# Kernel tuning notes

Hardware: AMD Instinct MI355X
Metric: run time of the kernel (lower is better)

## Reference

```python
import jax, jax.numpy as jnp
import numpy as np

B, H, W = 2, 512, 512
C2, HEADS = 128, 8
EPS_NORM = 1e-12  # torch F.normalize eps


def conv2d(x, w, groups=1):
    # x: NCHW, w: OIHW, stride 1, SAME padding
    return jax.lax.conv_general_dilated(
        x, w, window_strides=(1, 1), padding='SAME',
        dimension_numbers=('NCHW', 'OIHW', 'NCHW'),
        feature_group_count=groups)


def setup_inputs() -> dict:
    key = jax.random.key(0)
    ks = jax.random.split(key, 7)
    x = jax.random.normal(ks[0], (B, 2, H, W), dtype=jnp.float32)
    e = jax.random.normal(ks[1], (B, 1, H, W), dtype=jnp.float32)
    # imhead: 1x1 conv 2 -> 2*C2, then 3x3 depthwise conv on 2*C2 channels
    w_conv1 = jax.random.normal(ks[2], (2 * C2, 2, 1, 1), dtype=jnp.float32) * 0.5
    w_dw = jax.random.normal(ks[3], (2 * C2, 1, 3, 3), dtype=jnp.float32) * 0.2
    # ehead: 3x3 conv 1 -> C2 (groups=1)
    w_ehead = jax.random.normal(ks[4], (C2, 1, 3, 3), dtype=jnp.float32) * 0.2
    # project_out: 1x1 conv C2 -> 2
    w_proj = jax.random.normal(ks[5], (2, C2, 1, 1), dtype=jnp.float32) * 0.1
    a1 = jnp.ones((HEADS, 1, 1), dtype=jnp.float32)
    return {"x": x, "e": e, "w_conv1": w_conv1, "w_dw": w_dw,
            "w_ehead": w_ehead, "w_proj": w_proj, "a1": a1}


def l2norm_lastdim(t):
    n = jnp.sqrt(jnp.sum(t * t, axis=-1, keepdims=True))
    return t / jnp.maximum(n, EPS_NORM)


def reference(x, e, w_conv1, w_dw, w_ehead, w_proj, a1):
    b, _, h, w = x.shape
    # NOTE: attHead_image.forward never applies its LayerNorm, so neither do we.
    q1 = conv2d(x, w_conv1)                 # (B, 2*C2, H, W)
    q1 = conv2d(q1, w_dw, groups=2 * C2)    # depthwise 3x3
    k_eg = conv2d(e, w_ehead)               # (B, C2, H, W)
    q_im, v_im = jnp.split(q1, 2, axis=1)   # each (B, C2, H, W)

    def heads(t):  # (B, C2, H, W) -> (B, head, c, H*W)
        return t.reshape(b, HEADS, C2 // HEADS, h * w)

    q = l2norm_lastdim(heads(q_im))
    k = l2norm_lastdim(heads(k_eg))
    v = heads(v_im)

    # channel-wise attention: (B, head, c, c)
    attn = jnp.einsum('bhcn,bhdn->bhcd', q, k) * a1
    attn = jax.nn.softmax(attn, axis=-1)
    out = jnp.einsum('bhcd,bhdn->bhcn', attn, v)  # (B, head, c, H*W)
    out = out.reshape(b, C2, h, w)
    return x + conv2d(out, w_proj)
```

## Files before the change

### kernel.cpp

```cpp
#include <hip/hip_runtime.h>

#define IMG 512
#define NPIX (IMG*IMG)

__global__ __launch_bounds__(256,2) void gram_kernel(const float* __restrict__ x,
                                                     const float* __restrict__ e,
                                                     float* __restrict__ part){
  const int dyi = blockIdx.y;
  const int dy  = dyi - 2;
  const int b   = blockIdx.z;
  const int half= threadIdx.x >> 7;
  const int cx  = (threadIdx.x & 127) << 2;
  const int r0  = (blockIdx.x << 4) + (half << 3);
  const float* x0 = x + (size_t)b*2*NPIX;
  const float* x1 = x0 + NPIX;
  const float* ep = e + (size_t)b*NPIX;

  float acc[6][5];
#pragma unroll
  for (int t=0;t<6;t++)
#pragma unroll
    for (int j=0;j<5;j++) acc[t][j]=0.f;

  const bool okL = (cx >= 4), okR = (cx < 508);

#pragma unroll 2
  for (int s=0;s<8;s++){
    const int r = r0+s;
    const float4 a0 = *(const float4*)(x0 + r*IMG + cx);
    const float4 a1 = *(const float4*)(x1 + r*IMG + cx);
    const float4 aE = *(const float4*)(ep + r*IMG + cx);
    const int rb = r+dy;
    if ((unsigned)rb < (unsigned)IMG){
      const float* p0 = x0 + rb*IMG;
      const float* p1 = x1 + rb*IMG;
      const float* pe = ep + rb*IMG;
      float w0[8], w1[8], wE[8];
      {
        const float4 z = make_float4(0.f,0.f,0.f,0.f);
        float4 L,M,R;
        L = okL ? *(const float4*)(p0+cx-4) : z;
        M = *(const float4*)(p0+cx);
        R = okR ? *(const float4*)(p0+cx+4) : z;
        w0[0]=L.z;w0[1]=L.w;w0[2]=M.x;w0[3]=M.y;w0[4]=M.z;w0[5]=M.w;w0[6]=R.x;w0[7]=R.y;
        L = okL ? *(const float4*)(p1+cx-4) : z;
        M = *(const float4*)(p1+cx);
        R = okR ? *(const float4*)(p1+cx+4) : z;
        w1[0]=L.z;w1[1]=L.w;w1[2]=M.x;w1[3]=M.y;w1[4]=M.z;w1[5]=M.w;w1[6]=R.x;w1[7]=R.y;
        L = okL ? *(const float4*)(pe+cx-4) : z;
        M = *(const float4*)(pe+cx);
        R = okR ? *(const float4*)(pe+cx+4) : z;
        wE[0]=L.z;wE[1]=L.w;wE[2]=M.x;wE[3]=M.y;wE[4]=M.z;wE[5]=M.w;wE[6]=R.x;wE[7]=R.y;
      }
#pragma unroll
      for (int j=0;j<5;j++){
        acc[0][j] += a0.x*w0[j] + a0.y*w0[j+1] + a0.z*w0[j+2] + a0.w*w0[j+3];
        acc[1][j] += a0.x*w1[j] + a0.y*w1[j+1] + a0.z*w1[j+2] + a0.w*w1[j+3];
        acc[2][j] += a1.x*w1[j] + a1.y*w1[j+1] + a1.z*w1[j+2] + a1.w*w1[j+3];
        acc[3][j] += a0.x*wE[j] + a0.y*wE[j+1] + a0.z*wE[j+2] + a0.w*wE[j+3];
        acc[4][j] += a1.x*wE[j] + a1.y*wE[j+1] + a1.z*wE[j+2] + a1.w*wE[j+3];
        acc[5][j] += aE.x*wE[j] + aE.y*wE[j+1] + aE.z*wE[j+2] + aE.w*wE[j+3];
      }
    }
  }

  __shared__ float red[4][30];
  const int wv   = threadIdx.x >> 6;
  const int lane = threadIdx.x & 63;
#pragma unroll
  for (int t=0;t<6;t++)
#pragma unroll
    for (int j=0;j<5;j++){
      float v = acc[t][j];
      for (int off=32; off; off>>=1) v += __shfl_down(v, off);
      if (lane==0) red[wv][t*5+j] = v;
    }
  __syncthreads();
  if (threadIdx.x < 30){
    const int g = b*5 + dyi;
    part[(size_t)((g*32)+blockIdx.x)*32 + threadIdx.x] =
      red[0][threadIdx.x]+red[1][threadIdx.x]+red[2][threadIdx.x]+red[3][threadIdx.x];
  }
}

__global__ __launch_bounds__(256,1) void attn_kernel(const float* __restrict__ part,
                                                     const float* __restrict__ w_conv1,
                                                     const float* __restrict__ w_dw,
                                                     const float* __restrict__ w_ehead,
                                                     const float* __restrict__ w_proj,
                                                     const float* __restrict__ a1,
                                                     float* __restrict__ AB){
  const int tid = threadIdx.x;
  __shared__ float Lred[2][150];
  __shared__ float we_lds[128][9];
  __shared__ float nk_lds[2][128];
  __shared__ float attn_lds[2][8][16][16];
  __shared__ float M_lds[2][2][128];

  for (int i=tid; i<300; i+=256){
    const int bb=i/150, li=i%150;
    const int t=li/25, lag=li%25, dyi=lag/5, dxi=lag%5;
    const int g = bb*5+dyi;
    const float* p = part + (size_t)(g*32)*32 + t*5+dxi;
    float s=0.f;
#pragma unroll
    for (int j=0;j<32;j++) s += p[j*32];
    Lred[bb][li]=s;
  }
  if (tid<128){
#pragma unroll
    for (int t=0;t<9;t++) we_lds[tid][t]=w_ehead[tid*9+t];
  }
  __syncthreads();

  const int b=tid>>7, h=(tid>>4)&7, c=tid&15;
  const int C=h*16+c;
  const float* Lb  = Lred[b];
  const float* L00=Lb, *L01=Lb+25, *L11=Lb+50, *L0e=Lb+75, *L1e=Lb+100, *Lee=Lb+125;

  float u[9], v[9];
  {
    const float wa=w_conv1[C*2+0], wb=w_conv1[C*2+1];
#pragma unroll
    for (int t=0;t<9;t++){ const float wd=w_dw[C*9+t]; u[t]=wd*wa; v[t]=wd*wb; }
  }
  float nq2=0.f, nk2=0.f;
#pragma unroll
  for (int t=0;t<9;t++){
    const int ty=t/3, tx=t%3;
#pragma unroll
    for (int t2=0;t2<9;t2++){
      const int dy=t2/3-ty, dx=t2%3-tx;
      const int di=( dy+2)*5+( dx+2);
      const int dj=(-dy+2)*5+(-dx+2);
      nq2 += u[t]*u[t2]*L00[di] + u[t]*v[t2]*L01[di] + v[t]*u[t2]*L01[dj] + v[t]*v[t2]*L11[di];
      nk2 += we_lds[C][t]*we_lds[C][t2]*Lee[di];
    }
  }
  nk_lds[b][C]=sqrtf(nk2);
  float P[9];
#pragma unroll
  for (int t2=0;t2<9;t2++){
    float s=0.f;
    const int t2y=t2/3, t2x=t2%3;
#pragma unroll
    for (int t=0;t<9;t++){
      const int di=(t2y-t/3+2)*5+(t2x-t%3+2);
      s += u[t]*L0e[di] + v[t]*L1e[di];
    }
    P[t2]=s;
  }
  __syncthreads();
  const float inv_nq = 1.f/fmaxf(sqrtf(nq2), 1e-12f);
  const float a1h=a1[h];
  float lg[16], mx=-1e30f;
#pragma unroll
  for (int d=0; d<16; d++){
    float S=0.f;
#pragma unroll
    for (int t2=0;t2<9;t2++) S += P[t2]*we_lds[h*16+d][t2];
    const float l = S*inv_nq/fmaxf(nk_lds[b][h*16+d],1e-12f)*a1h;
    lg[d]=l; mx=fmaxf(mx,l);
  }
  float sum=0.f;
#pragma unroll
  for (int d=0;d<16;d++){ lg[d]=expf(lg[d]-mx); sum+=lg[d]; }
  const float inv=1.f/sum;
#pragma unroll
  for (int d=0;d<16;d++) attn_lds[b][h][c][d]=lg[d]*inv;
  __syncthreads();
  for (int i=tid;i<512;i+=256){
    const int G=i&127, o=(i>>7)&1, bb=i>>8;
    const int hh=G>>4, dd=G&15;
    float s=0.f;
#pragma unroll
    for (int cc=0;cc<16;cc++) s += w_proj[o*128 + hh*16+cc]*attn_lds[bb][hh][cc][dd];
    M_lds[bb][o][G]=s;
  }
  __syncthreads();
  if (tid<36){
    const int t=tid%9, o=(tid/9)&1, bb=tid/18;
    float sa=0.f, sb=0.f;
    for (int G=0;G<128;G++){
      const float m=M_lds[bb][o][G];
      const float wd=w_dw[(128+G)*9+t];
      sa += m*wd*w_conv1[(128+G)*2+0];
      sb += m*wd*w_conv1[(128+G)*2+1];
    }
    AB[(bb*2+o)*9+t]      = sa;
    AB[72 + (bb*2+o)*9+t] = sb;
  }
}

__global__ __launch_bounds__(256,1) void out_kernel(const float* __restrict__ x,
                                                    const float* __restrict__ AB,
                                                    float* __restrict__ out){
  const int idx = blockIdx.x*256 + threadIdx.x;
  const int b  = idx >> 16;
  const int y  = (idx >> 7) & (IMG-1);
  const int xc = (idx & 127) << 2;
  const float* x0 = x + (size_t)b*2*NPIX;
  const float* x1 = x0 + NPIX;

  float A0[9],A1[9],B0[9],B1[9];
#pragma unroll
  for (int t=0;t<9;t++){
    A0[t]=AB[(b*2+0)*9+t];      A1[t]=AB[(b*2+1)*9+t];
    B0[t]=AB[72+(b*2+0)*9+t];   B1[t]=AB[72+(b*2+1)*9+t];
  }
  float v0[3][6], v1[3][6];
#pragma unroll
  for (int r=0;r<3;r++){
    const int yy=y-1+r;
    if ((unsigned)yy < (unsigned)IMG){
      const float* p0=x0+(size_t)yy*IMG;
      const float* p1=x1+(size_t)yy*IMG;
      const float4 m0=*(const float4*)(p0+xc);
      const float4 m1=*(const float4*)(p1+xc);
      v0[r][1]=m0.x; v0[r][2]=m0.y; v0[r][3]=m0.z; v0[r][4]=m0.w;
      v1[r][1]=m1.x; v1[r][2]=m1.y; v1[r][3]=m1.z; v1[r][4]=m1.w;
      v0[r][0]=(xc>0)?p0[xc-1]:0.f;        v1[r][0]=(xc>0)?p1[xc-1]:0.f;
      v0[r][5]=(xc+4<IMG)?p0[xc+4]:0.f;    v1[r][5]=(xc+4<IMG)?p1[xc+4]:0.f;
    } else {
#pragma unroll
      for (int c2=0;c2<6;c2++){v0[r][c2]=0.f;v1[r][c2]=0.f;}
    }
  }
  float res0[4], res1[4];
#pragma unroll
  for (int i=0;i<4;i++){
    float s0=v0[1][i+1];
    float s1=v1[1][i+1];
#pragma unroll
    for (int t=0;t<9;t++){
      const int ty=t/3, tx=t%3;
      const float g0=v0[ty][i+tx], g1=v1[ty][i+tx];
      s0 += A0[t]*g0 + B0[t]*g1;
      s1 += A1[t]*g0 + B1[t]*g1;
    }
    res0[i]=s0; res1[i]=s1;
  }
  float* o0p = out + ((size_t)(b*2+0)*IMG + y)*IMG + xc;
  float* o1p = out + ((size_t)(b*2+1)*IMG + y)*IMG + xc;
  *(float4*)o0p = make_float4(res0[0],res0[1],res0[2],res0[3]);
  *(float4*)o1p = make_float4(res1[0],res1[1],res1[2],res1[3]);
}

extern "C" void kernel_launch(void* const* d_in, const int* in_sizes, int n_in,
                              void* d_out, int out_size, void* d_ws, size_t ws_size,
                              hipStream_t stream){
  const float* x       = (const float*)d_in[0];
  const float* e       = (const float*)d_in[1];
  const float* w_conv1 = (const float*)d_in[2];
  const float* w_dw    = (const float*)d_in[3];
  const float* w_ehead = (const float*)d_in[4];
  const float* w_proj  = (const float*)d_in[5];
  const float* a1      = (const float*)d_in[6];
  float* ws   = (float*)d_ws;
  float* part = ws;
  float* AB   = ws + 10240;
  float* out  = (float*)d_out;

  hipLaunchKernelGGL(gram_kernel, dim3(32,5,2), dim3(256), 0, stream, x, e, part);
  hipLaunchKernelGGL(attn_kernel, dim3(1),      dim3(256), 0, stream, part,
                     w_conv1, w_dw, w_ehead, w_proj, a1, AB);
  hipLaunchKernelGGL(out_kernel,  dim3(512),    dim3(256), 0, stream, x, AB, out);
}
```

Measured before the change: 44.82 us.

## Fuse gram, attention and output kernels into one persistent kernel with grid barrier

```diff
diff --git a/kernel.cpp b/kernel.cpp
--- a/kernel.cpp
+++ b/kernel.cpp
@@ -2,248 +2,259 @@
 
 #define IMG 512
 #define NPIX (IMG*IMG)
-
-__global__ __launch_bounds__(256,2) void gram_kernel(const float* __restrict__ x,
-                                                     const float* __restrict__ e,
-                                                     float* __restrict__ part){
-  const int dyi = blockIdx.y;
-  const int dy  = dyi - 2;
-  const int b   = blockIdx.z;
-  const int half= threadIdx.x >> 7;
-  const int cx  = (threadIdx.x & 127) << 2;
-  const int r0  = (blockIdx.x << 4) + (half << 3);
-  const float* x0 = x + (size_t)b*2*NPIX;
-  const float* x1 = x0 + NPIX;
-  const float* ep = e + (size_t)b*NPIX;
-
-  float acc[6][5];
-#pragma unroll
-  for (int t=0;t<6;t++)
-#pragma unroll
-    for (int j=0;j<5;j++) acc[t][j]=0.f;
-
-  const bool okL = (cx >= 4), okR = (cx < 508);
-
-#pragma unroll 2
-  for (int s=0;s<8;s++){
-    const int r = r0+s;
-    const float4 a0 = *(const float4*)(x0 + r*IMG + cx);
-    const float4 a1 = *(const float4*)(x1 + r*IMG + cx);
-    const float4 aE = *(const float4*)(ep + r*IMG + cx);
-    const int rb = r+dy;
-    if ((unsigned)rb < (unsigned)IMG){
-      const float* p0 = x0 + rb*IMG;
-      const float* p1 = x1 + rb*IMG;
-      const float* pe = ep + rb*IMG;
-      float w0[8], w1[8], wE[8];
-      {
-        const float4 z = make_float4(0.f,0.f,0.f,0.f);
-        float4 L,M,R;
-        L = okL ? *(const float4*)(p0+cx-4) : z;
-        M = *(const float4*)(p0+cx);
-        R = okR ? *(const float4*)(p0+cx+4) : z;
-        w0[0]=L.z;w0[1]=L.w;w0[2]=M.x;w0[3]=M.y;w0[4]=M.z;w0[5]=M.w;w0[6]=R.x;w0[7]=R.y;
-        L = okL ? *(const float4*)(p1+cx-4) : z;
-        M = *(const float4*)(p1+cx);
-        R = okR ? *(const float4*)(p1+cx+4) : z;
-        w1[0]=L.z;w1[1]=L.w;w1[2]=M.x;w1[3]=M.y;w1[4]=M.z;w1[5]=M.w;w1[6]=R.x;w1[7]=R.y;
-        L = okL ? *(const float4*)(pe+cx-4) : z;
-        M = *(const float4*)(pe+cx);
-        R = okR ? *(const float4*)(pe+cx+4) : z;
-        wE[0]=L.z;wE[1]=L.w;wE[2]=M.x;wE[3]=M.y;wE[4]=M.z;wE[5]=M.w;wE[6]=R.x;wE[7]=R.y;
-      }
-#pragma unroll
-      for (int j=0;j<5;j++){
-        acc[0][j] += a0.x*w0[j] + a0.y*w0[j+1] + a0.z*w0[j+2] + a0.w*w0[j+3];
-        acc[1][j] += a0.x*w1[j] + a0.y*w1[j+1] + a0.z*w1[j+2] + a0.w*w1[j+3];
-        acc[2][j] += a1.x*w1[j] + a1.y*w1[j+1] + a1.z*w1[j+2] + a1.w*w1[j+3];
-        acc[3][j] += a0.x*wE[j] + a0.y*wE[j+1] + a0.z*wE[j+2] + a0.w*wE[j+3];
-        acc[4][j] += a1.x*wE[j] + a1.y*wE[j+1] + a1.z*wE[j+2] + a1.w*wE[j+3];
-        acc[5][j] += aE.x*wE[j] + aE.y*wE[j+1] + aE.z*wE[j+2] + aE.w*wE[j+3];
-      }
-    }
-  }
+#define NBLK 256
+
+__global__ __launch_bounds__(256,2) void fused_kernel(
+    const float* __restrict__ x, const float* __restrict__ e,
+    const float* __restrict__ w_conv1, const float* __restrict__ w_dw,
+    const float* __restrict__ w_ehead, const float* __restrict__ w_proj,
+    const float* __restrict__ a1,
+    float* __restrict__ part, unsigned int* __restrict__ bar,
+    float* __restrict__ out)
+{
+  const int blk = blockIdx.x;
+  const int tid = threadIdx.x;
 
   __shared__ float red[4][30];
-  const int wv   = threadIdx.x >> 6;
-  const int lane = threadIdx.x & 63;
-#pragma unroll
-  for (int t=0;t<6;t++)
-#pragma unroll
-    for (int j=0;j<5;j++){
-      float v = acc[t][j];
-      for (int off=32; off; off>>=1) v += __shfl_down(v, off);
-      if (lane==0) red[wv][t*5+j] = v;
-    }
-  __syncthreads();
-  if (threadIdx.x < 30){
-    const int g = b*5 + dyi;
-    part[(size_t)((g*32)+blockIdx.x)*32 + threadIdx.x] =
-      red[0][threadIdx.x]+red[1][threadIdx.x]+red[2][threadIdx.x]+red[3][threadIdx.x];
-  }
-}
-
-__global__ __launch_bounds__(256,1) void attn_kernel(const float* __restrict__ part,
-                                                     const float* __restrict__ w_conv1,
-                                                     const float* __restrict__ w_dw,
-                                                     const float* __restrict__ w_ehead,
-                                                     const float* __restrict__ w_proj,
-                                                     const float* __restrict__ a1,
-                                                     float* __restrict__ AB){
-  const int tid = threadIdx.x;
   __shared__ float Lred[2][150];
   __shared__ float we_lds[128][9];
   __shared__ float nk_lds[2][128];
   __shared__ float attn_lds[2][8][16][16];
   __shared__ float M_lds[2][2][128];
-
-  for (int i=tid; i<300; i+=256){
-    const int bb=i/150, li=i%150;
-    const int t=li/25, lag=li%25, dyi=lag/5, dxi=lag%5;
-    const int g = bb*5+dyi;
-    const float* p = part + (size_t)(g*32)*32 + t*5+dxi;
-    float s=0.f;
-#pragma unroll
-    for (int j=0;j<32;j++) s += p[j*32];
-    Lred[bb][li]=s;
-  }
-  if (tid<128){
-#pragma unroll
-    for (int t=0;t<9;t++) we_lds[tid][t]=w_ehead[tid*9+t];
+  __shared__ float AB_lds[2][2][2][9];
+
+  for (int u = blk; u < 320; u += NBLK){
+    const int bx  = u & 31;
+    const int dyi = (u >> 5) % 5;
+    const int dy  = dyi - 2;
+    const int b   = u / 160;
+    const int half= tid >> 7;
+    const int cx  = (tid & 127) << 2;
+    const int r0  = (bx << 4) + (half << 3);
+    const float* x0 = x + (size_t)b*2*NPIX;
+    const float* x1 = x0 + NPIX;
+    const float* ep = e + (size_t)b*NPIX;
+
+    float acc[6][5];
+#pragma unroll
+    for (int t=0;t<6;t++)
+#pragma unroll
+      for (int j=0;j<5;j++) acc[t][j]=0.f;
+
+    const bool okL = (cx >= 4), okR = (cx < 508);
+
+#pragma unroll 2
+    for (int s=0;s<8;s++){
+      const int r = r0+s;
+      const float4 a0 = *(const float4*)(x0 + r*IMG + cx);
+      const float4 a1v= *(const float4*)(x1 + r*IMG + cx);
+      const float4 aE = *(const float4*)(ep + r*IMG + cx);
+      const int rb = r+dy;
+      if ((unsigned)rb < (unsigned)IMG){
+        const float* p0 = x0 + rb*IMG;
+        const float* p1 = x1 + rb*IMG;
+        const float* pe = ep + rb*IMG;
+        float w0[8], w1[8], wE[8];
+        {
+          const float4 z = make_float4(0.f,0.f,0.f,0.f);
+          float4 L,M,R;
+          L = okL ? *(const float4*)(p0+cx-4) : z;
+          M = *(const float4*)(p0+cx);
+          R = okR ? *(const float4*)(p0+cx+4) : z;
+          w0[0]=L.z;w0[1]=L.w;w0[2]=M.x;w0[3]=M.y;w0[4]=M.z;w0[5]=M.w;w0[6]=R.x;w0[7]=R.y;
+          L = okL ? *(const float4*)(p1+cx-4) : z;
+          M = *(const float4*)(p1+cx);
+          R = okR ? *(const float4*)(p1+cx+4) : z;
+          w1[0]=L.z;w1[1]=L.w;w1[2]=M.x;w1[3]=M.y;w1[4]=M.z;w1[5]=M.w;w1[6]=R.x;w1[7]=R.y;
+          L = okL ? *(const float4*)(pe+cx-4) : z;
+          M = *(const float4*)(pe+cx);
+          R = okR ? *(const float4*)(pe+cx+4) : z;
+          wE[0]=L.z;wE[1]=L.w;wE[2]=M.x;wE[3]=M.y;wE[4]=M.z;wE[5]=M.w;wE[6]=R.x;wE[7]=R.y;
+        }
+#pragma unroll
+        for (int j=0;j<5;j++){
+          acc[0][j] += a0.x*w0[j] + a0.y*w0[j+1] + a0.z*w0[j+2] + a0.w*w0[j+3];
+          acc[1][j] += a0.x*w1[j] + a0.y*w1[j+1] + a0.z*w1[j+2] + a0.w*w1[j+3];
+          acc[2][j] += a1v.x*w1[j] + a1v.y*w1[j+1] + a1v.z*w1[j+2] + a1v.w*w1[j+3];
+          acc[3][j] += a0.x*wE[j] + a0.y*wE[j+1] + a0.z*wE[j+2] + a0.w*wE[j+3];
+          acc[4][j] += a1v.x*wE[j] + a1v.y*wE[j+1] + a1v.z*wE[j+2] + a1v.w*wE[j+3];
+          acc[5][j] += aE.x*wE[j] + aE.y*wE[j+1] + aE.z*wE[j+2] + aE.w*wE[j+3];
+        }
+      }
+    }
+
+    const int wv   = tid >> 6;
+    const int lane = tid & 63;
+#pragma unroll
+    for (int t=0;t<6;t++)
+#pragma unroll
+      for (int j=0;j<5;j++){
+        float v = acc[t][j];
+        for (int off=32; off; off>>=1) v += __shfl_down(v, off);
+        if (lane==0) red[wv][t*5+j] = v;
+      }
+    __syncthreads();
+    if (tid < 30)
+      part[(size_t)u*32 + tid] = red[0][tid]+red[1][tid]+red[2][tid]+red[3][tid];
+    __syncthreads();
+  }
+
+  if (tid == 0){
+    __threadfence();
+    __hip_atomic_fetch_add(bar, 1u, __ATOMIC_RELEASE, __HIP_MEMORY_SCOPE_AGENT);
+    while (__hip_atomic_load(bar, __ATOMIC_ACQUIRE, __HIP_MEMORY_SCOPE_AGENT) < NBLK) { }
   }
   __syncthreads();
 
-  const int b=tid>>7, h=(tid>>4)&7, c=tid&15;
-  const int C=h*16+c;
-  const float* Lb  = Lred[b];
-  const float* L00=Lb, *L01=Lb+25, *L11=Lb+50, *L0e=Lb+75, *L1e=Lb+100, *Lee=Lb+125;
-
-  float u[9], v[9];
   {
-    const float wa=w_conv1[C*2+0], wb=w_conv1[C*2+1];
-#pragma unroll
-    for (int t=0;t<9;t++){ const float wd=w_dw[C*9+t]; u[t]=wd*wa; v[t]=wd*wb; }
-  }
-  float nq2=0.f, nk2=0.f;
-#pragma unroll
-  for (int t=0;t<9;t++){
-    const int ty=t/3, tx=t%3;
-#pragma unroll
-    for (int t2=0;t2<9;t2++){
-      const int dy=t2/3-ty, dx=t2%3-tx;
-      const int di=( dy+2)*5+( dx+2);
-      const int dj=(-dy+2)*5+(-dx+2);
-      nq2 += u[t]*u[t2]*L00[di] + u[t]*v[t2]*L01[di] + v[t]*u[t2]*L01[dj] + v[t]*v[t2]*L11[di];
-      nk2 += we_lds[C][t]*we_lds[C][t2]*Lee[di];
-    }
-  }
-  nk_lds[b][C]=sqrtf(nk2);
-  float P[9];
-#pragma unroll
-  for (int t2=0;t2<9;t2++){
-    float s=0.f;
-    const int t2y=t2/3, t2x=t2%3;
-#pragma unroll
-    for (int t=0;t<9;t++){
-      const int di=(t2y-t/3+2)*5+(t2x-t%3+2);
-      s += u[t]*L0e[di] + v[t]*L1e[di];
-    }
-    P[t2]=s;
-  }
-  __syncthreads();
-  const float inv_nq = 1.f/fmaxf(sqrtf(nq2), 1e-12f);
-  const float a1h=a1[h];
-  float lg[16], mx=-1e30f;
-#pragma unroll
-  for (int d=0; d<16; d++){
-    float S=0.f;
-#pragma unroll
-    for (int t2=0;t2<9;t2++) S += P[t2]*we_lds[h*16+d][t2];
-    const float l = S*inv_nq/fmaxf(nk_lds[b][h*16+d],1e-12f)*a1h;
-    lg[d]=l; mx=fmaxf(mx,l);
-  }
-  float sum=0.f;
-#pragma unroll
-  for (int d=0;d<16;d++){ lg[d]=expf(lg[d]-mx); sum+=lg[d]; }
-  const float inv=1.f/sum;
-#pragma unroll
-  for (int d=0;d<16;d++) attn_lds[b][h][c][d]=lg[d]*inv;
-  __syncthreads();
-  for (int i=tid;i<512;i+=256){
-    const int G=i&127, o=(i>>7)&1, bb=i>>8;
-    const int hh=G>>4, dd=G&15;
-    float s=0.f;
-#pragma unroll
-    for (int cc=0;cc<16;cc++) s += w_proj[o*128 + hh*16+cc]*attn_lds[bb][hh][cc][dd];
-    M_lds[bb][o][G]=s;
-  }
-  __syncthreads();
-  if (tid<36){
-    const int t=tid%9, o=(tid/9)&1, bb=tid/18;
-    float sa=0.f, sb=0.f;
-    for (int G=0;G<128;G++){
-      const float m=M_lds[bb][o][G];
-      const float wd=w_dw[(128+G)*9+t];
-      sa += m*wd*w_conv1[(128+G)*2+0];
-      sb += m*wd*w_conv1[(128+G)*2+1];
-    }
-    AB[(bb*2+o)*9+t]      = sa;
-    AB[72 + (bb*2+o)*9+t] = sb;
-  }
-}
-
-__global__ __launch_bounds__(256,1) void out_kernel(const float* __restrict__ x,
-                                                    const float* __restrict__ AB,
-                                                    float* __restrict__ out){
-  const int idx = blockIdx.x*256 + threadIdx.x;
-  const int b  = idx >> 16;
-  const int y  = (idx >> 7) & (IMG-1);
-  const int xc = (idx & 127) << 2;
-  const float* x0 = x + (size_t)b*2*NPIX;
-  const float* x1 = x0 + NPIX;
-
-  float A0[9],A1[9],B0[9],B1[9];
-#pragma unroll
-  for (int t=0;t<9;t++){
-    A0[t]=AB[(b*2+0)*9+t];      A1[t]=AB[(b*2+1)*9+t];
-    B0[t]=AB[72+(b*2+0)*9+t];   B1[t]=AB[72+(b*2+1)*9+t];
-  }
-  float v0[3][6], v1[3][6];
-#pragma unroll
-  for (int r=0;r<3;r++){
-    const int yy=y-1+r;
-    if ((unsigned)yy < (unsigned)IMG){
-      const float* p0=x0+(size_t)yy*IMG;
-      const float* p1=x1+(size_t)yy*IMG;
-      const float4 m0=*(const float4*)(p0+xc);
-      const float4 m1=*(const float4*)(p1+xc);
-      v0[r][1]=m0.x; v0[r][2]=m0.y; v0[r][3]=m0.z; v0[r][4]=m0.w;
-      v1[r][1]=m1.x; v1[r][2]=m1.y; v1[r][3]=m1.z; v1[r][4]=m1.w;
-      v0[r][0]=(xc>0)?p0[xc-1]:0.f;        v1[r][0]=(xc>0)?p1[xc-1]:0.f;
-      v0[r][5]=(xc+4<IMG)?p0[xc+4]:0.f;    v1[r][5]=(xc+4<IMG)?p1[xc+4]:0.f;
-    } else {
-#pragma unroll
-      for (int c2=0;c2<6;c2++){v0[r][c2]=0.f;v1[r][c2]=0.f;}
-    }
-  }
-  float res0[4], res1[4];
-#pragma unroll
-  for (int i=0;i<4;i++){
-    float s0=v0[1][i+1];
-    float s1=v1[1][i+1];
+    for (int i=tid; i<300; i+=256){
+      const int bb=i/150, li=i%150;
+      const int t=li/25, lag=li%25, dyi=lag/5, dxi=lag%5;
+      const int u0 = bb*160 + dyi*32;
+      const float* p = part + (size_t)u0*32 + t*5+dxi;
+      float s=0.f;
+#pragma unroll
+      for (int j=0;j<32;j++) s += p[j*32];
+      Lred[bb][li]=s;
+    }
+    if (tid<128){
+#pragma unroll
+      for (int t=0;t<9;t++) we_lds[tid][t]=w_ehead[tid*9+t];
+    }
+    __syncthreads();
+
+    const int b=tid>>7, h=(tid>>4)&7, c=tid&15;
+    const int C=h*16+c;
+    const float* Lb  = Lred[b];
+    const float* L00=Lb, *L01=Lb+25, *L11=Lb+50, *L0e=Lb+75, *L1e=Lb+100, *Lee=Lb+125;
+
+    float u[9], v[9];
+    {
+      const float wa=w_conv1[C*2+0], wb=w_conv1[C*2+1];
+#pragma unroll
+      for (int t=0;t<9;t++){ const float wd=w_dw[C*9+t]; u[t]=wd*wa; v[t]=wd*wb; }
+    }
+    float nq2=0.f, nk2=0.f;
 #pragma unroll
     for (int t=0;t<9;t++){
       const int ty=t/3, tx=t%3;
-      const float g0=v0[ty][i+tx], g1=v1[ty][i+tx];
-      s0 += A0[t]*g0 + B0[t]*g1;
-      s1 += A1[t]*g0 + B1[t]*g1;
-    }
-    res0[i]=s0; res1[i]=s1;
-  }
-  float* o0p = out + ((size_t)(b*2+0)*IMG + y)*IMG + xc;
-  float* o1p = out + ((size_t)(b*2+1)*IMG + y)*IMG + xc;
-  *(float4*)o0p = make_float4(res0[0],res0[1],res0[2],res0[3]);
-  *(float4*)o1p = make_float4(res1[0],res1[1],res1[2],res1[3]);
+#pragma unroll
+      for (int t2=0;t2<9;t2++){
+        const int dy=t2/3-ty, dx=t2%3-tx;
+        const int di=( dy+2)*5+( dx+2);
+        const int dj=(-dy+2)*5+(-dx+2);
+        nq2 += u[t]*u[t2]*L00[di] + u[t]*v[t2]*L01[di] + v[t]*u[t2]*L01[dj] + v[t]*v[t2]*L11[di];
+        nk2 += we_lds[C][t]*we_lds[C][t2]*Lee[di];
+      }
+    }
+    nk_lds[b][C]=sqrtf(nk2);
+    float P[9];
+#pragma unroll
+    for (int t2=0;t2<9;t2++){
+      float s=0.f;
+      const int t2y=t2/3, t2x=t2%3;
+#pragma unroll
+      for (int t=0;t<9;t++){
+        const int di=(t2y-t/3+2)*5+(t2x-t%3+2);
+        s += u[t]*L0e[di] + v[t]*L1e[di];
+      }
+      P[t2]=s;
+    }
+    __syncthreads();
+    const float inv_nq = 1.f/fmaxf(sqrtf(nq2), 1e-12f);
+    const float a1h=a1[h];
+    float lg[16], mx=-1e30f;
+#pragma unroll
+    for (int d=0; d<16; d++){
+      float S=0.f;
+#pragma unroll
+      for (int t2=0;t2<9;t2++) S += P[t2]*we_lds[h*16+d][t2];
+      const float l = S*inv_nq/fmaxf(nk_lds[b][h*16+d],1e-12f)*a1h;
+      lg[d]=l; mx=fmaxf(mx,l);
+    }
+    float sum=0.f;
+#pragma unroll
+    for (int d=0;d<16;d++){ lg[d]=expf(lg[d]-mx); sum+=lg[d]; }
+    const float inv=1.f/sum;
+#pragma unroll
+    for (int d=0;d<16;d++) attn_lds[b][h][c][d]=lg[d]*inv;
+    __syncthreads();
+    for (int i=tid;i<512;i+=256){
+      const int G=i&127, o=(i>>7)&1, bb=i>>8;
+      const int hh=G>>4, dd=G&15;
+      float s=0.f;
+#pragma unroll
+      for (int cc=0;cc<16;cc++) s += w_proj[o*128 + hh*16+cc]*attn_lds[bb][hh][cc][dd];
+      M_lds[bb][o][G]=s;
+    }
+    __syncthreads();
+    if (tid<36){
+      const int t=tid%9, o=(tid/9)&1, bb=tid/18;
+      float sa=0.f, sb=0.f;
+      for (int G=0;G<128;G++){
+        const float m=M_lds[bb][o][G];
+        const float wd=w_dw[(128+G)*9+t];
+        sa += m*wd*w_conv1[(128+G)*2+0];
+        sb += m*wd*w_conv1[(128+G)*2+1];
+      }
+      AB_lds[bb][o][0][t] = sa;
+      AB_lds[bb][o][1][t] = sb;
+    }
+    __syncthreads();
+  }
+
+#pragma unroll
+  for (int it=0; it<2; ++it){
+    const int idx = it*65536 + blk*256 + tid;
+    const int b  = idx >> 16;
+    const int y  = (idx >> 7) & (IMG-1);
+    const int xc = (idx & 127) << 2;
+    const float* x0 = x + (size_t)b*2*NPIX;
+    const float* x1 = x0 + NPIX;
+
+    float A0[9],A1[9],B0[9],B1[9];
+#pragma unroll
+    for (int t=0;t<9;t++){
+      A0[t]=AB_lds[b][0][0][t];  A1[t]=AB_lds[b][1][0][t];
+      B0[t]=AB_lds[b][0][1][t];  B1[t]=AB_lds[b][1][1][t];
+    }
+    float v0[3][6], v1[3][6];
+#pragma unroll
+    for (int r=0;r<3;r++){
+      const int yy=y-1+r;
+      if ((unsigned)yy < (unsigned)IMG){
+        const float* p0=x0+(size_t)yy*IMG;
+        const float* p1=x1+(size_t)yy*IMG;
+        const float4 m0=*(const float4*)(p0+xc);
+        const float4 m1=*(const float4*)(p1+xc);
+        v0[r][1]=m0.x; v0[r][2]=m0.y; v0[r][3]=m0.z; v0[r][4]=m0.w;
+        v1[r][1]=m1.x; v1[r][2]=m1.y; v1[r][3]=m1.z; v1[r][4]=m1.w;
+        v0[r][0]=(xc>0)?p0[xc-1]:0.f;        v1[r][0]=(xc>0)?p1[xc-1]:0.f;
+        v0[r][5]=(xc+4<IMG)?p0[xc+4]:0.f;    v1[r][5]=(xc+4<IMG)?p1[xc+4]:0.f;
+      } else {
+#pragma unroll
+        for (int c2=0;c2<6;c2++){v0[r][c2]=0.f;v1[r][c2]=0.f;}
+      }
+    }
+    float res0[4], res1[4];
+#pragma unroll
+    for (int i=0;i<4;i++){
+      float s0=v0[1][i+1];
+      float s1=v1[1][i+1];
+#pragma unroll
+      for (int t=0;t<9;t++){
+        const int ty=t/3, tx=t%3;
+        const float g0=v0[ty][i+tx], g1=v1[ty][i+tx];
+        s0 += A0[t]*g0 + B0[t]*g1;
+        s1 += A1[t]*g0 + B1[t]*g1;
+      }
+      res0[i]=s0; res1[i]=s1;
+    }
+    float* o0p = out + ((size_t)(b*2+0)*IMG + y)*IMG + xc;
+    float* o1p = out + ((size_t)(b*2+1)*IMG + y)*IMG + xc;
+    *(float4*)o0p = make_float4(res0[0],res0[1],res0[2],res0[3]);
+    *(float4*)o1p = make_float4(res1[0],res1[1],res1[2],res1[3]);
+  }
 }
 
 extern "C" void kernel_launch(void* const* d_in, const int* in_sizes, int n_in,
@@ -258,11 +269,10 @@
   const float* a1      = (const float*)d_in[6];
   float* ws   = (float*)d_ws;
   float* part = ws;
-  float* AB   = ws + 10240;
+  unsigned int* bar = (unsigned int*)(ws + 10240);
   float* out  = (float*)d_out;
 
-  hipLaunchKernelGGL(gram_kernel, dim3(32,5,2), dim3(256), 0, stream, x, e, part);
-  hipLaunchKernelGGL(attn_kernel, dim3(1),      dim3(256), 0, stream, part,
-                     w_conv1, w_dw, w_ehead, w_proj, a1, AB);
-  hipLaunchKernelGGL(out_kernel,  dim3(512),    dim3(256), 0, stream, x, AB, out);
+  hipMemsetAsync(bar, 0, sizeof(unsigned int), stream);
+  hipLaunchKernelGGL(fused_kernel, dim3(NBLK), dim3(256), 0, stream,
+                     x, e, w_conv1, w_dw, w_ehead, w_proj, a1, part, bar, out);
 }
```

Measured after the change: 84.32 us. 88.1% more time.
